# Optimization experiments

Measured on AMD Instinct MI355X. Metric: run time of the kernel, lower is better.

The kernel has to match this reference:

```python
import jax, jax.numpy as jnp
import numpy as np

B, T, C, H = 4, 2048, 1024, 16
D = C // H  # head_size = 64


def _layernorm(x, g, b, eps=1e-5):
    mu = jnp.mean(x, axis=-1, keepdims=True)
    var = jnp.var(x, axis=-1, keepdims=True)
    return (x - mu) * jax.lax.rsqrt(var + eps) * g + b


def setup_inputs() -> dict:
    key = jax.random.key(0)
    ks = jax.random.split(key, 12)
    s = 0.02
    return {
        "x": jax.random.normal(ks[0], (B, T, C), dtype=jnp.float32),
        "Wq": jax.random.normal(ks[1], (C, C), dtype=jnp.float32) * s,
        "Wk": jax.random.normal(ks[2], (C, C), dtype=jnp.float32) * s,
        "Wv": jax.random.normal(ks[3], (C, C), dtype=jnp.float32) * s,
        "Wo": jax.random.normal(ks[4], (C, C), dtype=jnp.float32) * s,
        "bo": jnp.zeros((C,), dtype=jnp.float32),
        "ln1_g": jnp.ones((C,), dtype=jnp.float32),
        "ln1_b": jnp.zeros((C,), dtype=jnp.float32),
        "ln2_g": jnp.ones((C,), dtype=jnp.float32),
        "ln2_b": jnp.zeros((C,), dtype=jnp.float32),
        "W1": jax.random.normal(ks[5], (C, 4 * C), dtype=jnp.float32) * s,
        "b1": jnp.zeros((4 * C,), dtype=jnp.float32),
        "W2": jax.random.normal(ks[6], (4 * C, C), dtype=jnp.float32) * s,
        "b2": jnp.zeros((C,), dtype=jnp.float32),
    }


def reference(x, Wq, Wk, Wv, Wo, bo, ln1_g, ln1_b, ln2_g, ln2_b, W1, b1, W2, b2):
    # --- self-attention branch (pre-LN) ---
    h = _layernorm(x, ln1_g, ln1_b)
    q = (h @ Wq).reshape(B, T, H, D)
    k = (h @ Wk).reshape(B, T, H, D)
    v = (h @ Wv).reshape(B, T, H, D)
    scores = jnp.einsum("bqhd,bkhd->bhqk", q, k) * (D ** -0.5)
    causal = jnp.tril(jnp.ones((T, T), dtype=bool))
    scores = jnp.where(causal, scores, -jnp.inf)
    attn = jax.nn.softmax(scores, axis=-1)  # dropout=0 in eval
    out = jnp.einsum("bhqk,bkhd->bqhd", attn, v).reshape(B, T, C)
    x = x + (out @ Wo + bo)
    # --- feed-forward branch (pre-LN) ---
    h2 = _layernorm(x, ln2_g, ln2_b)
    ff = jax.nn.relu(h2 @ W1 + b1) @ W2 + b2
    return x + ff
```

## Files before the change

### kernel.cpp

```cpp
#include <hip/hip_runtime.h>
#include <hip/hip_bf16.h>
#include <math.h>

#define Bsz 4
#define Tsz 2048
#define Csz 1024
#define Hsz 16
#define Dsz 64
#define Msz (Bsz * Tsz)

typedef __attribute__((ext_vector_type(8))) __bf16 bf16x8;
typedef __attribute__((ext_vector_type(2))) __bf16 bf16x2;
typedef __attribute__((ext_vector_type(4))) float f32x4;

#define GLOBAL_AS __attribute__((address_space(1)))
#define LDS_AS    __attribute__((address_space(3)))


__device__ __forceinline__ float block_sum256(float v, float* sh) {
#pragma unroll
    for (int o = 32; o > 0; o >>= 1) v += __shfl_down(v, o, 64);
    int lane = threadIdx.x & 63, w = threadIdx.x >> 6;
    __syncthreads();
    if (lane == 0) sh[w] = v;
    __syncthreads();
    return sh[0] + sh[1] + sh[2] + sh[3];
}


__global__ __launch_bounds__(256) void layernorm_bf16(const float* __restrict__ x,
                                                      const float* __restrict__ g,
                                                      const float* __restrict__ b,
                                                      __bf16* __restrict__ out) {
    __shared__ float sh[4];
    const int row = blockIdx.x;
    const float* xr = x + (size_t)row * Csz;
    float v[4];
    float s = 0.f, ss = 0.f;
#pragma unroll
    for (int i = 0; i < 4; i++) {
        v[i] = xr[threadIdx.x + i * 256];
        s += v[i];
        ss += v[i] * v[i];
    }
    float tot = block_sum256(s, sh);
    float mean = tot * (1.0f / Csz);
    float tot2 = block_sum256(ss, sh);
    float var = tot2 * (1.0f / Csz) - mean * mean;
    float inv = rsqrtf(var + 1e-5f);
    __bf16* orow = out + (size_t)row * Csz;
#pragma unroll
    for (int i = 0; i < 4; i++) {
        int c = threadIdx.x + i * 256;
        orow[c] = (__bf16)((v[i] - mean) * inv * g[c] + b[c]);
    }
}


__global__ __launch_bounds__(256) void transpose_bf16(const float* __restrict__ W,
                                                      __bf16* __restrict__ Wt,
                                                      int K, int N) {
    __shared__ float t[32][33];
    const int k0 = blockIdx.y * 32, n0 = blockIdx.x * 32;
    const int c = threadIdx.x & 31, r8 = threadIdx.x >> 5;
#pragma unroll
    for (int it = 0; it < 4; it++) {
        int r = r8 + it * 8;
        t[r][c] = W[(size_t)(k0 + r) * N + n0 + c];
    }
    __syncthreads();
#pragma unroll
    for (int it = 0; it < 4; it++) {
        int r = r8 + it * 8;
        Wt[(size_t)(n0 + r) * K + k0 + c] = (__bf16)t[c][r];
    }
}

__global__ __launch_bounds__(256) void transpose4_bf16(const float* __restrict__ Wa,
                                                       const float* __restrict__ Wb,
                                                       const float* __restrict__ Wc,
                                                       const float* __restrict__ Wd,
                                                       __bf16* __restrict__ Ta,
                                                       __bf16* __restrict__ Tb,
                                                       __bf16* __restrict__ Tc,
                                                       __bf16* __restrict__ Td) {
    __shared__ float t[32][33];
    const float* W = (blockIdx.z == 0) ? Wa : (blockIdx.z == 1) ? Wb : (blockIdx.z == 2) ? Wc : Wd;
    __bf16* Wt = (blockIdx.z == 0) ? Ta : (blockIdx.z == 1) ? Tb : (blockIdx.z == 2) ? Tc : Td;
    const int k0 = blockIdx.y * 32, n0 = blockIdx.x * 32;
    const int c = threadIdx.x & 31, r8 = threadIdx.x >> 5;
#pragma unroll
    for (int it = 0; it < 4; it++) {
        int r = r8 + it * 8;
        t[r][c] = W[(size_t)(k0 + r) * Csz + n0 + c];
    }
    __syncthreads();
#pragma unroll
    for (int it = 0; it < 4; it++) {
        int r = r8 + it * 8;
        Wt[(size_t)(n0 + r) * Csz + k0 + c] = (__bf16)t[c][r];
    }
}


__global__ __launch_bounds__(256) void gemm_bf16(const __bf16* __restrict__ A,
                                                 const __bf16* __restrict__ Bt,
                                                 float* __restrict__ Cf,
                                                 float* __restrict__ Cf2,
                                                 __bf16* __restrict__ Cb,
                                                 int M, int N, int K, int ld,
                                                 const float* __restrict__ bias,
                                                 const float* __restrict__ resid,
                                                 int do_relu) {
    __shared__ __bf16 As[128 * 64];
    __shared__ __bf16 Bs[128 * 64];

    const int tid = threadIdx.x;
    const int lane = tid & 63;
    const int w = tid >> 6;
    const int rowBase = blockIdx.y * 128;
    const int colBase = blockIdx.x * 128;
    const int wr = (w & 1) * 64;
    const int wc = (w >> 1) * 64;

    const __bf16* Ak = A + (size_t)blockIdx.z * K;
    const __bf16* Bk = Bt + (size_t)blockIdx.z * K;
    float* Cfu = Cf;
    const float* residu = resid;
    const float* biasu = bias;
    if (blockIdx.z == 1) { Cfu = Cf2; residu = nullptr; biasu = nullptr; }

    const int m16 = lane & 15;
    const int kg = lane >> 4;
    const int swz = m16 & 7;

    const int sr = lane >> 3;
    const int sc = lane & 7;
    const int gcs = sc ^ sr;

    f32x4 acc[4][4] = {};

    for (int k0 = 0; k0 < K; k0 += 64) {
        __syncthreads();
#pragma unroll
        for (int it = 0; it < 4; it++) {
            int lr = w * 32 + it * 8;
            const __bf16* ga = Ak + (size_t)(rowBase + lr + sr) * ld + k0 + gcs * 8;
            __builtin_amdgcn_global_load_lds((const GLOBAL_AS unsigned int*)ga,
                                             (LDS_AS unsigned int*)(As + lr * 64),
                                             16, 0, 0);
            const __bf16* gb = Bk + (size_t)(colBase + lr + sr) * ld + k0 + gcs * 8;
            __builtin_amdgcn_global_load_lds((const GLOBAL_AS unsigned int*)gb,
                                             (LDS_AS unsigned int*)(Bs + lr * 64),
                                             16, 0, 0);
        }
        __syncthreads();

#pragma unroll
        for (int s = 0; s < 2; s++) {
            const int slot = ((s * 4 + kg) ^ swz) * 8;
            bf16x8 af[4], bfv[4];
#pragma unroll
            for (int i = 0; i < 4; i++)
                af[i] = *(const bf16x8*)(As + (wr + i * 16 + m16) * 64 + slot);
#pragma unroll
            for (int j = 0; j < 4; j++)
                bfv[j] = *(const bf16x8*)(Bs + (wc + j * 16 + m16) * 64 + slot);
#pragma unroll
            for (int i = 0; i < 4; i++)
#pragma unroll
                for (int j = 0; j < 4; j++)
                    acc[i][j] = __builtin_amdgcn_mfma_f32_16x16x32_bf16(af[i], bfv[j], acc[i][j], 0, 0, 0);
        }
    }

    const int cn = lane & 15;
    const int rq = (lane >> 4) * 4;
    float bj[4];
#pragma unroll
    for (int j = 0; j < 4; j++)
        bj[j] = biasu ? biasu[colBase + wc + j * 16 + cn] : 0.f;

#pragma unroll
    for (int i = 0; i < 4; i++) {
#pragma unroll
        for (int r = 0; r < 4; r++) {
            int m = rowBase + wr + i * 16 + rq + r;
            size_t rowOff = (size_t)m * N;
#pragma unroll
            for (int j = 0; j < 4; j++) {
                int n = colBase + wc + j * 16 + cn;
                float v = acc[i][j][r] + bj[j];
                if (do_relu) v = fmaxf(v, 0.f);
                if (residu) v += residu[rowOff + n];
                if (Cfu) Cfu[rowOff + n] = v;
                if (Cb && blockIdx.z == 0) Cb[rowOff + n] = (__bf16)v;
            }
        }
    }
}


__global__ __launch_bounds__(256) void add_partial(float* __restrict__ out,
                                                   const float* __restrict__ p,
                                                   const float* __restrict__ b2) {
    size_t i = ((size_t)blockIdx.x * 256 + threadIdx.x) * 4;
    float4 o = *(float4*)(out + i);
    const float4 a = *(const float4*)(p + i);
    const float4 bb = *(const float4*)(b2 + (i & (Csz - 1)));
    o.x += a.x + bb.x;
    o.y += a.y + bb.y;
    o.z += a.z + bb.z;
    o.w += a.w + bb.w;
    *(float4*)(out + i) = o;
}


__global__ __launch_bounds__(256, 4) void attn_mfma(const __bf16* __restrict__ QKV,
                                                    __bf16* __restrict__ O) {
    __shared__ __bf16 Ks[64 * 64];
    __shared__ __bf16 Vt[64 * 72];
    __shared__ __bf16 Ps[128 * 72];

    const int tid = threadIdx.x;
    const int lane = tid & 63;
    const int w = tid >> 6;
    const int bh = blockIdx.x;
    const int b = bh >> 4, h = bh & 15;
    const int qt = (int)gridDim.y - 1 - (int)blockIdx.y;
    const int qbase = qt * 128;
    const int ld3C = 3 * Csz;

    const __bf16* Qg = QKV + (size_t)(b * Tsz) * ld3C + h * Dsz;
    const __bf16* Kg = Qg + Csz;
    const __bf16* Vg = Qg + 2 * Csz;

    const int m16 = lane & 15;
    const int kg = lane >> 4;
    const int rq = kg * 4;
    const int wrow = w * 32;
    const int swz = m16 & 7;

    bf16x8 aq[2][2];
#pragma unroll
    for (int i = 0; i < 2; i++)
#pragma unroll
        for (int s = 0; s < 2; s++)
            aq[i][s] = *(const bf16x8*)(Qg + (size_t)(qbase + wrow + i * 16 + m16) * ld3C + (s * 4 + kg) * 8);

    const int sr = lane >> 3;
    const int sc = lane & 7;
    const int gcs = sc ^ sr;

    const int kp = (lane & 31) * 2;
    const int dg = w * 2 + (lane >> 5);

    f32x4 Oacc[2][4];
    float l_part[2][4];
#pragma unroll
    for (int i = 0; i < 2; i++)
#pragma unroll
        for (int j = 0; j < 4; j++) Oacc[i][j] = (f32x4){0.f, 0.f, 0.f, 0.f};
#pragma unroll
    for (int i = 0; i < 2; i++)
#pragma unroll
        for (int r = 0; r < 4; r++) l_part[i][r] = 0.f;

    const float CEXP = 0.18033688f;

    const int nkt = 2 * qt + 2;
    for (int kt = 0; kt < nkt; kt++) {
        const int kbase = kt * 64;
        __syncthreads();

#pragma unroll
        for (int it = 0; it < 2; it++) {
            int lr = w * 16 + it * 8 + sr;
            const __bf16* src = Kg + (size_t)(kbase + lr) * ld3C + gcs * 8;
            __builtin_amdgcn_global_load_lds((const GLOBAL_AS unsigned int*)src,
                                             (LDS_AS unsigned int*)(Ks + (w * 16 + it * 8) * 64),
                                             16, 0, 0);
        }
        bf16x8 v0 = *(const bf16x8*)(Vg + (size_t)(kbase + kp) * ld3C + dg * 8);
        bf16x8 v1 = *(const bf16x8*)(Vg + (size_t)(kbase + kp + 1) * ld3C + dg * 8);
        __syncthreads();

        f32x4 S[2][4];
#pragma unroll
        for (int i = 0; i < 2; i++)
#pragma unroll
            for (int j = 0; j < 4; j++) S[i][j] = (f32x4){0.f, 0.f, 0.f, 0.f};
#pragma unroll
        for (int s = 0; s < 2; s++) {
            bf16x8 bk[4];
#pragma unroll
            for (int j = 0; j < 4; j++)
                bk[j] = *(const bf16x8*)(Ks + (j * 16 + m16) * 64 + (((s * 4 + kg) ^ swz) * 8));
#pragma unroll
            for (int i = 0; i < 2; i++)
#pragma unroll
                for (int j = 0; j < 4; j++)
                    S[i][j] = __builtin_amdgcn_mfma_f32_16x16x32_bf16(aq[i][s], bk[j], S[i][j], 0, 0, 0);
        }

        const bool domask = (kt >= 2 * qt);
#pragma unroll
        for (int i = 0; i < 2; i++) {
#pragma unroll
            for (int j = 0; j < 4; j++) {
#pragma unroll
                for (int r = 0; r < 4; r++) {
                    float arg = S[i][j][r] * CEXP;
                    if (domask && (kbase + j * 16 + m16 > qbase + wrow + i * 16 + rq + r))
                        arg = -INFINITY;
                    float e = exp2f(arg);
                    S[i][j][r] = e;
                    l_part[i][r] += e;
                }
            }
        }

#pragma unroll
        for (int i = 0; i < 2; i++)
#pragma unroll
            for (int j = 0; j < 4; j++)
#pragma unroll
                for (int r = 0; r < 4; r++)
                    Ps[(wrow + i * 16 + rq + r) * 72 + j * 16 + m16] = (__bf16)S[i][j][r];
#pragma unroll
        for (int e = 0; e < 8; e++) {
            bf16x2 pr;
            pr[0] = v0[e];
            pr[1] = v1[e];
            *(bf16x2*)(Vt + (dg * 8 + e) * 72 + kp) = pr;
        }
        __syncthreads();

#pragma unroll
        for (int s = 0; s < 2; s++) {
            bf16x8 ap[2], bv[4];
#pragma unroll
            for (int i = 0; i < 2; i++)
                ap[i] = *(const bf16x8*)(Ps + (wrow + i * 16 + m16) * 72 + s * 32 + kg * 8);
#pragma unroll
            for (int j = 0; j < 4; j++)
                bv[j] = *(const bf16x8*)(Vt + (j * 16 + m16) * 72 + s * 32 + kg * 8);
#pragma unroll
            for (int i = 0; i < 2; i++)
#pragma unroll
                for (int j = 0; j < 4; j++)
                    Oacc[i][j] = __builtin_amdgcn_mfma_f32_16x16x32_bf16(ap[i], bv[j], Oacc[i][j], 0, 0, 0);
        }
    }

#pragma unroll
    for (int i = 0; i < 2; i++) {
#pragma unroll
        for (int r = 0; r < 4; r++) {
            float l = l_part[i][r];
#pragma unroll
            for (int msk = 1; msk < 16; msk <<= 1) l += __shfl_xor(l, msk, 64);
            const float inv = 1.0f / l;
            const int qrow = qbase + wrow + i * 16 + rq + r;
            __bf16* orow = O + (size_t)(b * Tsz + qrow) * Csz + h * Dsz;
#pragma unroll
            for (int j = 0; j < 4; j++)
                orow[j * 16 + m16] = (__bf16)(Oacc[i][j][r] * inv);
        }
    }
}


extern "C" void kernel_launch(void* const* d_in, const int* in_sizes, int n_in,
                              void* d_out, int out_size, void* d_ws, size_t ws_size,
                              hipStream_t stream) {
    const float* x     = (const float*)d_in[0];
    const float* Wq    = (const float*)d_in[1];
    const float* Wk    = (const float*)d_in[2];
    const float* Wv    = (const float*)d_in[3];
    const float* Wo    = (const float*)d_in[4];
    const float* bo    = (const float*)d_in[5];
    const float* ln1_g = (const float*)d_in[6];
    const float* ln1_b = (const float*)d_in[7];
    const float* ln2_g = (const float*)d_in[8];
    const float* ln2_b = (const float*)d_in[9];
    const float* W1    = (const float*)d_in[10];
    const float* b1    = (const float*)d_in[11];
    const float* W2    = (const float*)d_in[12];
    const float* b2    = (const float*)d_in[13];
    float* out = (float*)d_out;

    const size_t MB = 1u << 20;
    char* w = (char*)d_ws;
    __bf16* h    = (__bf16*)(w + 0);
    __bf16* Wqkv = (__bf16*)(w + 16 * MB);
    __bf16* Wot  = (__bf16*)(w + 22 * MB);
    __bf16* W1t  = (__bf16*)(w + 24 * MB);
    __bf16* W2t  = (__bf16*)(w + 32 * MB);
    __bf16* QKVb = (__bf16*)(w + 40 * MB);
    __bf16* AO   = (__bf16*)(w + 88 * MB);
    __bf16* ff1  = (__bf16*)(w + 40 * MB);
    float*  p1   = (float*)(w + 0);

    transpose4_bf16<<<dim3(32, 32, 4), 256, 0, stream>>>(Wq, Wk, Wv, Wo,
                                                         Wqkv, Wqkv + 1024 * 1024, Wqkv + 2048 * 1024, Wot);
    transpose_bf16<<<dim3(4 * Csz / 32, Csz / 32), 256, 0, stream>>>(W1, W1t, Csz, 4 * Csz);
    transpose_bf16<<<dim3(Csz / 32, 4 * Csz / 32), 256, 0, stream>>>(W2, W2t, 4 * Csz, Csz);

    layernorm_bf16<<<Msz, 256, 0, stream>>>(x, ln1_g, ln1_b, h);
    gemm_bf16<<<dim3(3 * Csz / 128, Msz / 128), 256, 0, stream>>>(
        h, Wqkv, nullptr, nullptr, QKVb, Msz, 3 * Csz, Csz, Csz, nullptr, nullptr, 0);
    attn_mfma<<<dim3(Bsz * Hsz, Tsz / 128), 256, 0, stream>>>(QKVb, AO);
    gemm_bf16<<<dim3(Csz / 128, Msz / 128), 256, 0, stream>>>(
        AO, Wot, out, nullptr, nullptr, Msz, Csz, Csz, Csz, bo, x, 0);

    layernorm_bf16<<<Msz, 256, 0, stream>>>(out, ln2_g, ln2_b, h);
    gemm_bf16<<<dim3(4 * Csz / 128, Msz / 128), 256, 0, stream>>>(
        h, W1t, nullptr, nullptr, ff1, Msz, 4 * Csz, Csz, Csz, b1, nullptr, 1);
    gemm_bf16<<<dim3(Csz / 128, Msz / 128, 2), 256, 0, stream>>>(
        ff1, W2t, out, p1, nullptr, Msz, Csz, 2 * Csz, 4 * Csz, nullptr, out, 0);
    add_partial<<<Msz * Csz / 1024, 256, 0, stream>>>(out, p1, b2);
}
```

Before: 562.3 us.

## Store residual in bf16, split W2 GEMM into two launches, add grouped tile swizzle

The attention output projection now writes the residual stream as bf16 instead of fp32, and the second LayerNorm reads that bf16 tensor. The split-K FFN down-projection, which used a z-dimension partial buffer plus a separate add kernel, becomes two sequential GEMM launches. The second launch accumulates onto the output and adds the bias. The GEMM also remaps block indices into groups of 8 row-tiles for better L2 reuse. Rounding the residual to bf16 lowers precision, and the second K-half GEMM now runs serially instead of in the same grid.

Result: slower. 577.7 us (+2.7%).

```diff
diff --git a/kernel.cpp b/kernel.cpp
--- a/kernel.cpp
+++ b/kernel.cpp
@@ -28,20 +28,31 @@
 }
 
 
-__global__ __launch_bounds__(256) void layernorm_bf16(const float* __restrict__ x,
+__global__ __launch_bounds__(256) void layernorm_bf16(const float* __restrict__ xf,
+                                                      const __bf16* __restrict__ xb,
                                                       const float* __restrict__ g,
                                                       const float* __restrict__ b,
                                                       __bf16* __restrict__ out) {
     __shared__ float sh[4];
     const int row = blockIdx.x;
-    const float* xr = x + (size_t)row * Csz;
     float v[4];
     float s = 0.f, ss = 0.f;
-#pragma unroll
-    for (int i = 0; i < 4; i++) {
-        v[i] = xr[threadIdx.x + i * 256];
-        s += v[i];
-        ss += v[i] * v[i];
+    if (xf) {
+        const float* xr = xf + (size_t)row * Csz;
+#pragma unroll
+        for (int i = 0; i < 4; i++) {
+            v[i] = xr[threadIdx.x + i * 256];
+            s += v[i];
+            ss += v[i] * v[i];
+        }
+    } else {
+        const __bf16* xr = xb + (size_t)row * Csz;
+#pragma unroll
+        for (int i = 0; i < 4; i++) {
+            v[i] = (float)xr[threadIdx.x + i * 256];
+            s += v[i];
+            ss += v[i] * v[i];
+        }
     }
     float tot = block_sum256(s, sh);
     float mean = tot * (1.0f / Csz);
@@ -106,11 +117,11 @@
 __global__ __launch_bounds__(256) void gemm_bf16(const __bf16* __restrict__ A,
                                                  const __bf16* __restrict__ Bt,
                                                  float* __restrict__ Cf,
-                                                 float* __restrict__ Cf2,
                                                  __bf16* __restrict__ Cb,
                                                  int M, int N, int K, int ld,
                                                  const float* __restrict__ bias,
-                                                 const float* __restrict__ resid,
+                                                 const float* __restrict__ residf,
+                                                 const __bf16* __restrict__ residb,
                                                  int do_relu) {
     __shared__ __bf16 As[128 * 64];
     __shared__ __bf16 Bs[128 * 64];
@@ -118,17 +129,17 @@
     const int tid = threadIdx.x;
     const int lane = tid & 63;
     const int w = tid >> 6;
-    const int rowBase = blockIdx.y * 128;
-    const int colBase = blockIdx.x * 128;
+
+    const int gx = gridDim.x;
+    const int lin = blockIdx.x + gx * blockIdx.y;
+    const int t8 = lin >> 3;
+    const int bx = t8 % gx;
+    const int by = (lin & 7) + 8 * (t8 / gx);
+
+    const int rowBase = by * 128;
+    const int colBase = bx * 128;
     const int wr = (w & 1) * 64;
     const int wc = (w >> 1) * 64;
-
-    const __bf16* Ak = A + (size_t)blockIdx.z * K;
-    const __bf16* Bk = Bt + (size_t)blockIdx.z * K;
-    float* Cfu = Cf;
-    const float* residu = resid;
-    const float* biasu = bias;
-    if (blockIdx.z == 1) { Cfu = Cf2; residu = nullptr; biasu = nullptr; }
 
     const int m16 = lane & 15;
     const int kg = lane >> 4;
@@ -145,11 +156,11 @@
 #pragma unroll
         for (int it = 0; it < 4; it++) {
             int lr = w * 32 + it * 8;
-            const __bf16* ga = Ak + (size_t)(rowBase + lr + sr) * ld + k0 + gcs * 8;
+            const __bf16* ga = A + (size_t)(rowBase + lr + sr) * ld + k0 + gcs * 8;
             __builtin_amdgcn_global_load_lds((const GLOBAL_AS unsigned int*)ga,
                                              (LDS_AS unsigned int*)(As + lr * 64),
                                              16, 0, 0);
-            const __bf16* gb = Bk + (size_t)(colBase + lr + sr) * ld + k0 + gcs * 8;
+            const __bf16* gb = Bt + (size_t)(colBase + lr + sr) * ld + k0 + gcs * 8;
             __builtin_amdgcn_global_load_lds((const GLOBAL_AS unsigned int*)gb,
                                              (LDS_AS unsigned int*)(Bs + lr * 64),
                                              16, 0, 0);
@@ -179,7 +190,7 @@
     float bj[4];
 #pragma unroll
     for (int j = 0; j < 4; j++)
-        bj[j] = biasu ? biasu[colBase + wc + j * 16 + cn] : 0.f;
+        bj[j] = bias ? bias[colBase + wc + j * 16 + cn] : 0.f;
 
 #pragma unroll
     for (int i = 0; i < 4; i++) {
@@ -192,27 +203,13 @@
                 int n = colBase + wc + j * 16 + cn;
                 float v = acc[i][j][r] + bj[j];
                 if (do_relu) v = fmaxf(v, 0.f);
-                if (residu) v += residu[rowOff + n];
-                if (Cfu) Cfu[rowOff + n] = v;
-                if (Cb && blockIdx.z == 0) Cb[rowOff + n] = (__bf16)v;
+                if (residf) v += residf[rowOff + n];
+                if (residb) v += (float)residb[rowOff + n];
+                if (Cf) Cf[rowOff + n] = v;
+                if (Cb) Cb[rowOff + n] = (__bf16)v;
             }
         }
     }
-}
-
-
-__global__ __launch_bounds__(256) void add_partial(float* __restrict__ out,
-                                                   const float* __restrict__ p,
-                                                   const float* __restrict__ b2) {
-    size_t i = ((size_t)blockIdx.x * 256 + threadIdx.x) * 4;
-    float4 o = *(float4*)(out + i);
-    const float4 a = *(const float4*)(p + i);
-    const float4 bb = *(const float4*)(b2 + (i & (Csz - 1)));
-    o.x += a.x + bb.x;
-    o.y += a.y + bb.y;
-    o.z += a.z + bb.z;
-    o.w += a.w + bb.w;
-    *(float4*)(out + i) = o;
 }
 
 
@@ -400,24 +397,25 @@
     __bf16* QKVb = (__bf16*)(w + 40 * MB);
     __bf16* AO   = (__bf16*)(w + 88 * MB);
     __bf16* ff1  = (__bf16*)(w + 40 * MB);
-    float*  p1   = (float*)(w + 0);
+    __bf16* x2b  = (__bf16*)(w + 104 * MB);
 
     transpose4_bf16<<<dim3(32, 32, 4), 256, 0, stream>>>(Wq, Wk, Wv, Wo,
                                                          Wqkv, Wqkv + 1024 * 1024, Wqkv + 2048 * 1024, Wot);
     transpose_bf16<<<dim3(4 * Csz / 32, Csz / 32), 256, 0, stream>>>(W1, W1t, Csz, 4 * Csz);
     transpose_bf16<<<dim3(Csz / 32, 4 * Csz / 32), 256, 0, stream>>>(W2, W2t, 4 * Csz, Csz);
 
-    layernorm_bf16<<<Msz, 256, 0, stream>>>(x, ln1_g, ln1_b, h);
+    layernorm_bf16<<<Msz, 256, 0, stream>>>(x, nullptr, ln1_g, ln1_b, h);
     gemm_bf16<<<dim3(3 * Csz / 128, Msz / 128), 256, 0, stream>>>(
-        h, Wqkv, nullptr, nullptr, QKVb, Msz, 3 * Csz, Csz, Csz, nullptr, nullptr, 0);
+        h, Wqkv, nullptr, QKVb, Msz, 3 * Csz, Csz, Csz, nullptr, nullptr, nullptr, 0);
     attn_mfma<<<dim3(Bsz * Hsz, Tsz / 128), 256, 0, stream>>>(QKVb, AO);
     gemm_bf16<<<dim3(Csz / 128, Msz / 128), 256, 0, stream>>>(
-        AO, Wot, out, nullptr, nullptr, Msz, Csz, Csz, Csz, bo, x, 0);
-
-    layernorm_bf16<<<Msz, 256, 0, stream>>>(out, ln2_g, ln2_b, h);
+        AO, Wot, nullptr, x2b, Msz, Csz, Csz, Csz, bo, x, nullptr, 0);
+
+    layernorm_bf16<<<Msz, 256, 0, stream>>>(nullptr, x2b, ln2_g, ln2_b, h);
     gemm_bf16<<<dim3(4 * Csz / 128, Msz / 128), 256, 0, stream>>>(
-        h, W1t, nullptr, nullptr, ff1, Msz, 4 * Csz, Csz, Csz, b1, nullptr, 1);
-    gemm_bf16<<<dim3(Csz / 128, Msz / 128, 2), 256, 0, stream>>>(
-        ff1, W2t, out, p1, nullptr, Msz, Csz, 2 * Csz, 4 * Csz, nullptr, out, 0);
-    add_partial<<<Msz * Csz / 1024, 256, 0, stream>>>(out, p1, b2);
-}
+        h, W1t, nullptr, ff1, Msz, 4 * Csz, Csz, Csz, b1, nullptr, nullptr, 1);
+    gemm_bf16<<<dim3(Csz / 128, Msz / 128), 256, 0, stream>>>(
+        ff1, W2t, out, nullptr, Msz, Csz, 2 * Csz, 4 * Csz, nullptr, nullptr, x2b, 0);
+    gemm_bf16<<<dim3(Csz / 128, Msz / 128), 256, 0, stream>>>(
+        ff1 + 2 * Csz, W2t + 2 * Csz, out, nullptr, Msz, Csz, 2 * Csz, 4 * Csz, b2, out, nullptr, 0);
+}
```
